# Kernel tuning notes

Measured on AMD Instinct MI355X. Metric: run time of the kernel, lower is better.

Reference implementation:

```python
import jax, jax.numpy as jnp
import numpy as np

B, S, H = 32, 512, 768          # batch, encoder seq len, hidden size
W, G = 128, 4                   # max words per example, max tokens per word group
NH, HD, FF, NL, NLAB = 4, 192, 2048, 2, 6  # heads, head dim, ffn dim, layers, labels
EPS = 1e-5


def setup_inputs() -> dict:
    key = jax.random.key(0)
    ks = jax.random.split(key, 16)
    s = 0.02
    hidden = jax.random.normal(ks[0], (B, S, H), jnp.float32)
    word_token_idx = jax.random.randint(ks[1], (B, W, G), 0, S).astype(jnp.int32)
    glen = jax.random.randint(ks[2], (B, W), 1, G + 1)
    group_token_mask = jnp.arange(G)[None, None, :] < glen[:, :, None]  # [B,W,G] bool
    nwords = jax.random.randint(ks[3], (B,), W // 2, W + 1)
    word_valid = jnp.arange(W)[None, :] < nwords[:, None]               # [B,W] bool
    return {
        'hidden': hidden,
        'word_token_idx': word_token_idx,
        'group_token_mask': group_token_mask,
        'word_valid': word_valid,
        'qkv_w': jax.random.normal(ks[4], (NL, 3 * H, H), jnp.float32) * s,
        'qkv_b': jnp.zeros((NL, 3 * H), jnp.float32),
        'out_w': jax.random.normal(ks[5], (NL, H, H), jnp.float32) * s,
        'out_b': jnp.zeros((NL, H), jnp.float32),
        'ff1_w': jax.random.normal(ks[6], (NL, FF, H), jnp.float32) * s,
        'ff1_b': jnp.zeros((NL, FF), jnp.float32),
        'ff2_w': jax.random.normal(ks[7], (NL, H, FF), jnp.float32) * s,
        'ff2_b': jnp.zeros((NL, H), jnp.float32),
        'ln1_s': jnp.ones((NL, H), jnp.float32),
        'ln1_b': jnp.zeros((NL, H), jnp.float32),
        'ln2_s': jnp.ones((NL, H), jnp.float32),
        'ln2_b': jnp.zeros((NL, H), jnp.float32),
        'cls_w': jax.random.normal(ks[8], (NLAB, H), jnp.float32) * s,
        'cls_b': jnp.zeros((NLAB,), jnp.float32),
    }


def _ln(x, s, b):
    m = x.mean(-1, keepdims=True)
    v = ((x - m) ** 2).mean(-1, keepdims=True)
    return (x - m) * jax.lax.rsqrt(v + EPS) * s + b


def reference(hidden, word_token_idx, group_token_mask, word_valid,
              qkv_w, qkv_b, out_w, out_b, ff1_w, ff1_b, ff2_w, ff2_b,
              ln1_s, ln1_b, ln2_s, ln2_b, cls_w, cls_b):
    dt = hidden.dtype
    # ragged per-word gather + masked mean over each subword group: [B,W,G,H]
    gathered = jax.vmap(lambda h, i: h[i])(hidden, word_token_idx)
    gm = group_token_mask[..., None].astype(dt)
    wemb = (gathered * gm).sum(2) / jnp.maximum(gm.sum(2), 1.0)   # [B,W,H]
    # invalid (padded) words are zero, matching torch pad_sequence zero-padding
    wemb = wemb * word_valid[..., None].astype(dt)
    cls = hidden[:, 0, :]
    x = jnp.concatenate([cls[:, None, :], wemb], axis=1)          # [B, W+1, H]
    # key padding mask: True = padded position; CLS slot always valid
    pad = jnp.concatenate([jnp.zeros((B, 1), bool), ~word_valid], axis=1)
    neg = jnp.finfo(dt).min
    Lw = W + 1
    scale = 1.0 / np.sqrt(HD)
    for l in range(NL):  # 2 post-norm TransformerEncoder layers
        qkv = x @ qkv_w[l].T + qkv_b[l]
        q, k, v = jnp.split(qkv, 3, axis=-1)
        q = q.reshape(B, Lw, NH, HD).transpose(0, 2, 1, 3)
        k = k.reshape(B, Lw, NH, HD).transpose(0, 2, 1, 3)
        v = v.reshape(B, Lw, NH, HD).transpose(0, 2, 1, 3)
        scores = jnp.einsum('bhqd,bhkd->bhqk', q, k) * scale
        scores = jnp.where(pad[:, None, None, :], neg, scores)
        a = jax.nn.softmax(scores, axis=-1)
        ctx = jnp.einsum('bhqk,bhkd->bhqd', a, v).transpose(0, 2, 1, 3).reshape(B, Lw, H)
        attn = ctx @ out_w[l].T + out_b[l]
        x = _ln(x + attn, ln1_s[l], ln1_b[l])
        h1 = jax.nn.relu(x @ ff1_w[l].T + ff1_b[l])
        x = _ln(x + h1 @ ff2_w[l].T + ff2_b[l], ln2_s[l], ln2_b[l])
    pooled = x[:, 0, :]
    logits = pooled @ cls_w.T + cls_b
    return (logits, pooled)
```

## Files before the change

kernel.cpp:

```cpp
#include <hip/hip_runtime.h>
#include <hip/hip_bf16.h>
#include <math.h>

#define B_  32
#define S_  512
#define H_  768
#define W_  128
#define G_  4
#define LW  129
#define NH_ 4
#define HD_ 192
#define FF_ 2048
#define NL_ 2
#define NLAB_ 6
#define M_   (B_ * LW)
#define MPAD 4224
#define EPS_ 1e-5f
#define SCALE_ 0.07216878364870323f

#define TP 192
#define KP 160
#define KR 144
#define KLD 200
#define PLD 168

#define QW_SZ (3 * H_ * H_)
#define OW_SZ (H_ * H_)
#define F1_SZ (FF_ * H_)
#define F2_SZ (H_ * FF_)
#define WL_SZ (QW_SZ + OW_SZ + F1_SZ + F2_SZ)

typedef __bf16 bf16_8 __attribute__((ext_vector_type(8)));
typedef float  f32x4  __attribute__((ext_vector_type(4)));
typedef unsigned short ushort8_t __attribute__((ext_vector_type(8)));

__device__ __forceinline__ float b2f(unsigned short u) {
    union { unsigned int i; float f; } c; c.i = ((unsigned int)u) << 16; return c.f;
}
__device__ __forceinline__ unsigned short f2b(float f) {
    union { float f; unsigned int u; } c; c.f = f;
    unsigned int u = c.u;
    return (unsigned short)((u + 0x7FFFu + ((u >> 16) & 1u)) >> 16);
}

__device__ __forceinline__ float wave_sum(float v) {
#pragma unroll
    for (int off = 1; off < 64; off <<= 1) v += __shfl_xor(v, off, 64);
    return v;
}
__device__ __forceinline__ float wave_max(float v) {
#pragma unroll
    for (int off = 1; off < 64; off <<= 1) v = fmaxf(v, __shfl_xor(v, off, 64));
    return v;
}
__device__ __forceinline__ float block_sum(float v, float* red) {
    v = wave_sum(v);
    int wid = threadIdx.x >> 6, lane = threadIdx.x & 63;
    if (lane == 0) red[wid] = v;
    __syncthreads();
    float r = (red[0] + red[1]) + (red[2] + red[3]);
    __syncthreads();
    return r;
}

__global__ __launch_bounds__(256) void build_cvt_kernel(
    const float* __restrict__ hidden,
    const int*   __restrict__ wti,
    const int*   __restrict__ gmask,
    const int*   __restrict__ wvalid,
    unsigned short* __restrict__ xb,
    const float4* __restrict__ qw, const float4* __restrict__ ow,
    const float4* __restrict__ f1, const float4* __restrict__ f2,
    ushort4* __restrict__ dst)
{
    int bx = blockIdx.x;
    int tid = threadIdx.x;
    if (bx >= (LW + 3) * B_) {
        constexpr int WL4 = WL_SZ / 4;
        int i = (bx - (LW + 3) * B_) * 256 + tid;
        int l = (i < WL4) ? 0 : 1;
        int j = i - l * WL4;
        float4 v;
        if (j < QW_SZ / 4)                          v = qw[l * (QW_SZ / 4) + j];
        else if (j < (QW_SZ + OW_SZ) / 4)           v = ow[l * (OW_SZ / 4) + j - QW_SZ / 4];
        else if (j < (QW_SZ + OW_SZ + F1_SZ) / 4)   v = f1[l * (F1_SZ / 4) + j - (QW_SZ + OW_SZ) / 4];
        else                                        v = f2[l * (F2_SZ / 4) + j - (QW_SZ + OW_SZ + F1_SZ) / 4];
        ushort4 o; o.x = f2b(v.x); o.y = f2b(v.y); o.z = f2b(v.z); o.w = f2b(v.w);
        dst[i] = o;
        return;
    }
    int t = bx % (LW + 3);
    int b = bx / (LW + 3);
    if (t >= LW) {
        int pr = M_ + b * 3 + (t - LW);
        size_t xo = (size_t)pr * H_;
#pragma unroll
        for (int i = 0; i < 3; i++) xb[xo + tid + i * 256] = 0;
        return;
    }
    size_t xo = ((size_t)b * LW + t) * H_;
    if (t == 0) {
        const float* src = hidden + (size_t)b * S_ * H_;
#pragma unroll
        for (int i = 0; i < 3; i++) xb[xo + tid + i * 256] = f2b(src[tid + i * 256]);
    } else {
        int w = t - 1;
        int valid = wvalid[b * W_ + w];
        int ids[G_]; float msk[G_]; float cnt = 0.f;
#pragma unroll
        for (int g = 0; g < G_; g++) {
            ids[g] = wti[(b * W_ + w) * G_ + g];
            msk[g] = (gmask[(b * W_ + w) * G_ + g] != 0) ? 1.f : 0.f;
            cnt += msk[g];
        }
        float inv = valid ? (1.f / fmaxf(cnt, 1.f)) : 0.f;
#pragma unroll
        for (int i = 0; i < 3; i++) {
            int c = tid + i * 256;
            float a = 0.f;
#pragma unroll
            for (int g = 0; g < G_; g++)
                a += msk[g] * hidden[((size_t)b * S_ + ids[g]) * H_ + c];
            xb[xo + c] = f2b(a * inv);
        }
    }
}

template <int BM, int BN, int BK, int RELU, int OUTBF, int SWZ>
__global__ __launch_bounds__(256) void gemm_mfma(
    const unsigned short* __restrict__ A,
    const unsigned short* __restrict__ Bw,
    const float* __restrict__ bias,
    void* __restrict__ Cout,
    int N, int K, int ldc, int lda)
{
    constexpr int MI  = BM / 32;
    constexpr int NJ  = BN / 32;
    constexpr int CPR = BK / 8;
    constexpr int RPL = 2048 / BK;
    constexpr int SA  = BM * BK / 2048;
    constexpr int SB  = BN * BK / 2048;

    __shared__ __align__(16) unsigned short As[BM * BK];
    __shared__ __align__(16) unsigned short Bs[BN * BK];

    const int tid  = threadIdx.x;
    const int lane = tid & 63;
    const int wid  = tid >> 6;

    int bx = blockIdx.x, by = blockIdx.y;
    if (SWZ) {
        int nx = gridDim.x;
        int total = nx * gridDim.y;
        int id = by * nx + bx;
        int id2 = (id & 7) * (total >> 3) + (id >> 3);
        by = id2 / nx; bx = id2 - by * nx;
    }
    const int bm = by * BM;
    const int bn = bx * BN;

    const int wm = (wid & 1) * (BM / 2);
    const int wn = (wid >> 1) * (BN / 2);
    const int r  = lane & 15;
    const int q8 = lane >> 4;
    const int m8 = r & (CPR - 1);

    const int srow = tid / CPR;
    const int scol = (tid % CPR) ^ (srow & (CPR - 1));
    const unsigned short* Ag = A  + (size_t)(bm + srow) * lda + scol * 8;
    const unsigned short* Bg = Bw + (size_t)(bn + srow) * K + scol * 8;

    const bf16_8* Af = (const bf16_8*)As;
    const bf16_8* Bf = (const bf16_8*)Bs;
    int arow[MI], brow[NJ];
#pragma unroll
    for (int i = 0; i < MI; i++) arow[i] = (wm + i * 16 + r) * CPR;
#pragma unroll
    for (int j = 0; j < NJ; j++) brow[j] = (wn + j * 16 + r) * CPR;

    f32x4 acc[MI][NJ];
#pragma unroll
    for (int i = 0; i < MI; i++)
#pragma unroll
        for (int j = 0; j < NJ; j++) acc[i][j] = (f32x4){0.f, 0.f, 0.f, 0.f};

    for (int k0 = 0; k0 < K; k0 += BK) {
#pragma unroll
        for (int s = 0; s < SA; s++)
            __builtin_amdgcn_global_load_lds(
                (const __attribute__((address_space(1))) void*)(Ag + (size_t)(s * RPL) * lda + k0),
                (__attribute__((address_space(3))) void*)(As + s * 2048 + tid * 8), 16, 0, 0);
#pragma unroll
        for (int s = 0; s < SB; s++)
            __builtin_amdgcn_global_load_lds(
                (const __attribute__((address_space(1))) void*)(Bg + (size_t)(s * RPL) * K + k0),
                (__attribute__((address_space(3))) void*)(Bs + s * 2048 + tid * 8), 16, 0, 0);
        __syncthreads();
#pragma unroll
        for (int ks = 0; ks < BK / 32; ks++) {
            const int cc = (ks * 4 + q8) ^ m8;
            bf16_8 a[MI], b[NJ];
#pragma unroll
            for (int i = 0; i < MI; i++) a[i] = Af[arow[i] + cc];
#pragma unroll
            for (int j = 0; j < NJ; j++) b[j] = Bf[brow[j] + cc];
#pragma unroll
            for (int i = 0; i < MI; i++)
#pragma unroll
                for (int j = 0; j < NJ; j++)
                    acc[i][j] = __builtin_amdgcn_mfma_f32_16x16x32_bf16(a[i], b[j], acc[i][j], 0, 0, 0);
        }
        __syncthreads();
    }

    int col[NJ]; float bv[NJ];
#pragma unroll
    for (int j = 0; j < NJ; j++) { col[j] = bn + wn + j * 16 + r; bv[j] = bias[col[j]]; }
    const int row0 = bm + wm + ((lane >> 4) << 2);
#pragma unroll
    for (int i = 0; i < MI; i++) {
#pragma unroll
        for (int rg = 0; rg < 4; rg++) {
            size_t rowoff = (size_t)(row0 + i * 16 + rg) * ldc;
#pragma unroll
            for (int j = 0; j < NJ; j++) {
                float v = acc[i][j][rg] + bv[j];
                if (RELU) v = fmaxf(v, 0.f);
                if (OUTBF) ((unsigned short*)Cout)[rowoff + col[j]] = f2b(v);
                else       ((float*)Cout)[rowoff + col[j]] = v;
            }
        }
    }
}

__global__ __launch_bounds__(256) void vt_kernel(
    const unsigned short* __restrict__ qkv,
    unsigned short* __restrict__ vtb)
{
    __shared__ __align__(16) unsigned short Vs[KR * KLD];
    int bh = blockIdx.x;
    int b = bh >> 2, h = bh & 3;
    int tid = threadIdx.x;
    for (int c = tid; c < KR * 24; c += 256) {
        int t = c / 24, j = c - t * 24;
        ushort8_t v = (ushort8_t){0,0,0,0,0,0,0,0};
        if (t < LW)
            v = *(const ushort8_t*)(qkv + (size_t)(b * LW + t) * (3 * H_) + 2 * H_ + h * HD_ + j * 8);
        *(ushort8_t*)(&Vs[t * KLD + j * 8]) = v;
    }
    __syncthreads();
    size_t obase = (size_t)bh * (HD_ * KP);
    for (int c = tid; c < HD_ * (KP / 4); c += 256) {
        int d = c / (KP / 4), t0 = (c - d * (KP / 4)) * 4;
        ushort4 o;
        o.x = (t0 + 0 < KR) ? Vs[(t0 + 0) * KLD + d] : 0;
        o.y = (t0 + 1 < KR) ? Vs[(t0 + 1) * KLD + d] : 0;
        o.z = (t0 + 2 < KR) ? Vs[(t0 + 2) * KLD + d] : 0;
        o.w = (t0 + 3 < KR) ? Vs[(t0 + 3) * KLD + d] : 0;
        *(ushort4*)(&vtb[obase + (size_t)d * KP + t0]) = o;
    }
}

__global__ __launch_bounds__(256) void attn_fused_kernel(
    const unsigned short* __restrict__ qkv,
    const int*            __restrict__ wvalid,
    const unsigned short* __restrict__ vtb,
    unsigned short*       __restrict__ ctx)
{
    __shared__ __align__(16) unsigned short Ks[KR * KLD];
    __shared__ __align__(16) unsigned short Ps[64 * PLD];
    __shared__ float msk[KR];
    int mb = blockIdx.x;
    int bh = blockIdx.y;
    int b = bh >> 2, h = bh & 3;
    int tid = threadIdx.x, lane = tid & 63, wid = tid >> 6;
    int q = lane >> 4, r = lane & 15;

    for (int c = tid; c < KR * 24; c += 256) {
        int t = c / 24, j = c - t * 24;
        ushort8_t v = (ushort8_t){0,0,0,0,0,0,0,0};
        if (t < LW)
            v = *(const ushort8_t*)(qkv + (size_t)(b * LW + t) * (3 * H_) + H_ + h * HD_ + j * 8);
        *(ushort8_t*)(&Ks[t * KLD + j * 8]) = v;
    }
    if (tid < KR) {
        bool valid = (tid == 0) || (tid <= W_ && wvalid[b * W_ + tid - 1] != 0);
        msk[tid] = valid ? 0.f : -1e30f;
    }
    __syncthreads();

    const int lrow0 = wid * 16;
    const unsigned short* Qp = qkv + ((size_t)(b * LW) + mb * 64 + lrow0 + r) * (3 * H_) + h * HD_;

    f32x4 acc[9];
#pragma unroll
    for (int nt = 0; nt < 9; nt++) acc[nt] = (f32x4){0.f, 0.f, 0.f, 0.f};
    for (int ks = 0; ks < HD_ / 32; ks++) {
        bf16_8 a = *(const bf16_8*)(Qp + ks * 32 + q * 8);
#pragma unroll
        for (int nt = 0; nt < 9; nt++) {
            bf16_8 bfrag = *(const bf16_8*)(&Ks[(nt * 16 + r) * KLD + ks * 32 + q * 8]);
            acc[nt] = __builtin_amdgcn_mfma_f32_16x16x32_bf16(a, bfrag, acc[nt], 0, 0, 0);
        }
    }
    float mk[9];
#pragma unroll
    for (int nt = 0; nt < 9; nt++) mk[nt] = msk[nt * 16 + r];
#pragma unroll
    for (int rg = 0; rg < 4; rg++) {
        float v[9]; float mx = -1e30f;
#pragma unroll
        for (int nt = 0; nt < 9; nt++) { v[nt] = acc[nt][rg] * SCALE_ + mk[nt]; mx = fmaxf(mx, v[nt]); }
#pragma unroll
        for (int off = 1; off < 16; off <<= 1) mx = fmaxf(mx, __shfl_xor(mx, off, 64));
        float s = 0.f;
#pragma unroll
        for (int nt = 0; nt < 9; nt++) { v[nt] = __expf(v[nt] - mx); s += v[nt]; }
#pragma unroll
        for (int off = 1; off < 16; off <<= 1) s += __shfl_xor(s, off, 64);
        float inv = 1.f / s;
        int lr = lrow0 + q * 4 + rg;
#pragma unroll
        for (int nt = 0; nt < 9; nt++)
            Ps[lr * PLD + nt * 16 + r] = f2b(v[nt] * inv);
        Ps[lr * PLD + KR + r] = 0;
    }
    __syncthreads();

    const int wm = (wid & 1) * 32, wn = (wid >> 1) * 96;
    size_t vbase = (size_t)bh * (HD_ * KP);

    f32x4 pacc[2][6];
#pragma unroll
    for (int i = 0; i < 2; i++)
#pragma unroll
        for (int j = 0; j < 6; j++) pacc[i][j] = (f32x4){0.f, 0.f, 0.f, 0.f};

    for (int ks = 0; ks < KP / 32; ks++) {
        bf16_8 a[2], bb[6];
#pragma unroll
        for (int i = 0; i < 2; i++)
            a[i] = *(const bf16_8*)(&Ps[(wm + i * 16 + r) * PLD + ks * 32 + q * 8]);
#pragma unroll
        for (int j = 0; j < 6; j++)
            bb[j] = *(const bf16_8*)(vtb + vbase + (size_t)(wn + j * 16 + r) * KP + ks * 32 + q * 8);
#pragma unroll
        for (int i = 0; i < 2; i++)
#pragma unroll
            for (int j = 0; j < 6; j++)
                pacc[i][j] = __builtin_amdgcn_mfma_f32_16x16x32_bf16(a[i], bb[j], pacc[i][j], 0, 0, 0);
    }

#pragma unroll
    for (int i = 0; i < 2; i++) {
#pragma unroll
        for (int rg = 0; rg < 4; rg++) {
            int tl = mb * 64 + wm + i * 16 + q * 4 + rg;
            if (tl < LW) {
                size_t rowoff = (size_t)(b * LW + tl) * H_ + h * HD_;
#pragma unroll
                for (int j = 0; j < 6; j++)
                    ctx[rowoff + wn + j * 16 + r] = f2b(pacc[i][j][rg]);
            }
        }
    }
}

__global__ __launch_bounds__(256) void add_ln_kernel(
    unsigned short* __restrict__ xb, const unsigned short* __restrict__ res,
    const float* __restrict__ sc, const float* __restrict__ bi)
{
    __shared__ float red[4];
    int row = blockIdx.x;
    int tid = threadIdx.x;
    size_t base = (size_t)row * H_;
    float v[3];
    float sum = 0.f;
#pragma unroll
    for (int i = 0; i < 3; i++) {
        int c = tid + i * 256;
        float t = b2f(xb[base + c]) + b2f(res[base + c]);
        v[i] = t; sum += t;
    }
    sum = block_sum(sum, red);
    float mean = sum * (1.f / H_);
    float var = 0.f;
#pragma unroll
    for (int i = 0; i < 3; i++) { float d = v[i] - mean; var += d * d; }
    var = block_sum(var, red);
    float inv = rsqrtf(var * (1.f / H_) + EPS_);
#pragma unroll
    for (int i = 0; i < 3; i++) {
        int c = tid + i * 256;
        xb[base + c] = f2b((v[i] - mean) * inv * sc[c] + bi[c]);
    }
}

__global__ __launch_bounds__(256) void cls_attn_core2_kernel(
    const unsigned short* __restrict__ qrows,
    const unsigned short* __restrict__ qkvb,
    const int* __restrict__ wvalid,
    unsigned short* __restrict__ ctxc)
{
    __shared__ float qh[HD_];
    __shared__ float ps[LW];
    __shared__ float red[4];
    int b = blockIdx.x, h = blockIdx.y;
    int tid = threadIdx.x, lane = tid & 63, wid = tid >> 6;
    if (tid < HD_) qh[tid] = b2f(qrows[(size_t)b * H_ + h * HD_ + tid]);
    __syncthreads();
    float sc = -1e30f;
    if (tid < LW) {
        const unsigned short* kr = qkvb + (size_t)(b * LW + tid) * (3 * H_) + H_ + h * HD_;
        float acc = 0.f;
#pragma unroll
        for (int j = 0; j < HD_ / 8; j++) {
            ushort8_t k8 = *(const ushort8_t*)(kr + j * 8);
#pragma unroll
            for (int jj = 0; jj < 8; jj++) acc += qh[j * 8 + jj] * b2f(k8[jj]);
        }
        bool valid = (tid == 0) || (wvalid[b * W_ + tid - 1] != 0);
        sc = valid ? acc * SCALE_ : -1e30f;
    }
    float mx = wave_max(sc);
    if (lane == 0) red[wid] = mx;
    __syncthreads();
    mx = fmaxf(fmaxf(red[0], red[1]), fmaxf(red[2], red[3]));
    __syncthreads();
    float e = (tid < LW) ? __expf(sc - mx) : 0.f;
    float ssum = wave_sum(e);
    if (lane == 0) red[wid] = ssum;
    __syncthreads();
    ssum = (red[0] + red[1]) + (red[2] + red[3]);
    if (tid < LW) ps[tid] = e * (1.f / ssum);
    __syncthreads();
    if (tid < HD_) {
        const unsigned short* vb = qkvb + (size_t)(b * LW) * (3 * H_) + 2 * H_ + h * HD_ + tid;
        float cx = 0.f;
#pragma unroll 8
        for (int t = 0; t < LW; t++)
            cx += ps[t] * b2f(vb[(size_t)t * (3 * H_)]);
        ctxc[(size_t)b * H_ + h * HD_ + tid] = f2b(cx);
    }
}

__global__ __launch_bounds__(256) void cls_ln1_kernel(
    const unsigned short* __restrict__ proj,
    const unsigned short* __restrict__ xb,
    const float* __restrict__ sc, const float* __restrict__ bi,
    unsigned short* __restrict__ dst)
{
    __shared__ float red[4];
    int b = blockIdx.x;
    int tid = threadIdx.x;
    float v[3]; float sum = 0.f;
#pragma unroll
    for (int i = 0; i < 3; i++) {
        int c = tid + i * 256;
        float t = b2f(proj[(size_t)b * H_ + c]) + b2f(xb[(size_t)(b * LW) * H_ + c]);
        v[i] = t; sum += t;
    }
    sum = block_sum(sum, red);
    float mean = sum * (1.f / H_);
    float var = 0.f;
#pragma unroll
    for (int i = 0; i < 3; i++) { float d = v[i] - mean; var += d * d; }
    var = block_sum(var, red);
    float inv = rsqrtf(var * (1.f / H_) + EPS_);
#pragma unroll
    for (int i = 0; i < 3; i++) {
        int c = tid + i * 256;
        dst[(size_t)b * H_ + c] = f2b((v[i] - mean) * inv * sc[c] + bi[c]);
    }
}

__global__ __launch_bounds__(256) void cls_final_kernel(
    const unsigned short* __restrict__ proj,
    const unsigned short* __restrict__ resid,
    const float* __restrict__ ln2s, const float* __restrict__ ln2b,
    const float* __restrict__ cls_w, const float* __restrict__ cls_b,
    float* __restrict__ out)
{
    __shared__ float red[4];
    __shared__ float lred[4][NLAB_];
    int b = blockIdx.x;
    int tid = threadIdx.x, lane = tid & 63, wid = tid >> 6;
    size_t base = (size_t)b * H_;
    float v[3]; float sum = 0.f;
#pragma unroll
    for (int i = 0; i < 3; i++) {
        int c = tid + i * 256;
        float t = b2f(proj[base + c]) + b2f(resid[base + c]);
        v[i] = t; sum += t;
    }
    sum = block_sum(sum, red);
    float mean = sum * (1.f / H_);
    float var = 0.f;
#pragma unroll
    for (int i = 0; i < 3; i++) { float d = v[i] - mean; var += d * d; }
    var = block_sum(var, red);
    float rinv = rsqrtf(var * (1.f / H_) + EPS_);
    float f3[3];
#pragma unroll
    for (int i = 0; i < 3; i++) {
        int c = tid + i * 256;
        f3[i] = (v[i] - mean) * rinv * ln2s[c] + ln2b[c];
        out[B_ * NLAB_ + b * H_ + c] = f3[i];
    }
    float l6[NLAB_] = {0.f, 0.f, 0.f, 0.f, 0.f, 0.f};
#pragma unroll
    for (int i = 0; i < 3; i++) {
        int c = tid + i * 256;
#pragma unroll
        for (int w = 0; w < NLAB_; w++) l6[w] += f3[i] * cls_w[w * H_ + c];
    }
#pragma unroll
    for (int w = 0; w < NLAB_; w++) l6[w] = wave_sum(l6[w]);
    if (lane == 0) {
#pragma unroll
        for (int w = 0; w < NLAB_; w++) lred[wid][w] = l6[w];
    }
    __syncthreads();
    if (tid < NLAB_)
        out[b * NLAB_ + tid] = lred[0][tid] + lred[1][tid] + lred[2][tid] + lred[3][tid] + cls_b[tid];
}

extern "C" void kernel_launch(void* const* d_in, const int* in_sizes, int n_in,
                              void* d_out, int out_size, void* d_ws, size_t ws_size,
                              hipStream_t stream) {
    const float* hidden = (const float*)d_in[0];
    const int*   wti    = (const int*)d_in[1];
    const int*   gmask  = (const int*)d_in[2];
    const int*   wvalid = (const int*)d_in[3];
    const float* qkv_w  = (const float*)d_in[4];
    const float* qkv_b  = (const float*)d_in[5];
    const float* out_w  = (const float*)d_in[6];
    const float* out_b  = (const float*)d_in[7];
    const float* ff1_w  = (const float*)d_in[8];
    const float* ff1_b  = (const float*)d_in[9];
    const float* ff2_w  = (const float*)d_in[10];
    const float* ff2_b  = (const float*)d_in[11];
    const float* ln1_s  = (const float*)d_in[12];
    const float* ln1_b  = (const float*)d_in[13];
    const float* ln2_s  = (const float*)d_in[14];
    const float* ln2_b  = (const float*)d_in[15];
    const float* cls_w  = (const float*)d_in[16];
    const float* cls_b  = (const float*)d_in[17];
    float* out = (float*)d_out;

    const size_t XSZ = (size_t)MPAD * H_;
    const size_t ASZ = (size_t)128 * TP * KP;
    const size_t R64 = (size_t)64 * H_;
    unsigned short* U    = (unsigned short*)d_ws;
    unsigned short* vtb  = U;
    unsigned short* tmpb = U;
    unsigned short* qrows64 = U + 1 * R64;
    unsigned short* ctxc  = U + 2 * R64;
    unsigned short* xc64  = U + 3 * R64;
    unsigned short* tmp64 = U + 4 * R64;
    unsigned short* h1c   = U + 5 * R64;
    unsigned short* xb   = U + ASZ;
    unsigned short* ctxb = xb + XSZ;
    unsigned short* qkvb = ctxb + XSZ;
    unsigned short* wb   = qkvb + (size_t)MPAD * 3 * H_;

    build_cvt_kernel<<<(LW + 3) * B_ + 2 * WL_SZ / 4 / 256, 256, 0, stream>>>(
        hidden, wti, gmask, wvalid, xb,
        (const float4*)qkv_w, (const float4*)out_w,
        (const float4*)ff1_w, (const float4*)ff2_w, (ushort4*)wb);

    const int GM = MPAD / 64;

    {
        unsigned short* wbl = wb;
        gemm_mfma<64, 128, 64, 0, 1, 0><<<dim3(3 * H_ / 128, GM), 256, 0, stream>>>(
            xb, wbl, qkv_b, qkvb, 3 * H_, H_, 3 * H_, H_);
        vt_kernel<<<128, 256, 0, stream>>>(qkvb, vtb);
        attn_fused_kernel<<<dim3(3, 128), 256, 0, stream>>>(qkvb, wvalid, vtb, ctxb);
        gemm_mfma<64, 64, 64, 0, 1, 1><<<dim3(H_ / 64, GM), 256, 0, stream>>>(
            ctxb, wbl + QW_SZ, out_b, tmpb, H_, H_, H_, H_);
        add_ln_kernel<<<M_, 256, 0, stream>>>(xb, tmpb, ln1_s, ln1_b);
        gemm_mfma<64, 128, 64, 1, 1, 1><<<dim3(FF_ / 128, GM), 256, 0, stream>>>(
            xb, wbl + QW_SZ + OW_SZ, ff1_b, qkvb, FF_, H_, FF_, H_);
        gemm_mfma<64, 64, 64, 0, 1, 1><<<dim3(H_ / 64, GM), 256, 0, stream>>>(
            qkvb, wbl + QW_SZ + OW_SZ + F1_SZ, ff2_b, tmpb, H_, FF_, H_, FF_);
        add_ln_kernel<<<M_, 256, 0, stream>>>(xb, tmpb, ln2_s, ln2_b);
    }

    {
        unsigned short* wbl = wb + WL_SZ;
        gemm_mfma<64, 128, 64, 0, 1, 1><<<dim3(1536 / 128, GM), 256, 0, stream>>>(
            xb, wbl + (size_t)H_ * H_, qkv_b + 3 * H_ + H_, qkvb + H_, 2 * H_, H_, 3 * H_, H_);
        gemm_mfma<64, 128, 64, 0, 1, 0><<<dim3(H_ / 128, 1), 256, 0, stream>>>(
            xb, wbl, qkv_b + 3 * H_, qrows64, H_, H_, H_, LW * H_);
        cls_attn_core2_kernel<<<dim3(B_, NH_), 256, 0, stream>>>(
            qrows64, qkvb, wvalid, ctxc);
        gemm_mfma<64, 128, 64, 0, 1, 0><<<dim3(H_ / 128, 1), 256, 0, stream>>>(
            ctxc, wbl + QW_SZ, out_b + H_, tmp64, H_, H_, H_, H_);
        cls_ln1_kernel<<<B_, 256, 0, stream>>>(tmp64, xb, ln1_s + H_, ln1_b + H_, xc64);
        gemm_mfma<64, 128, 64, 1, 1, 0><<<dim3(FF_ / 128, 1), 256, 0, stream>>>(
            xc64, wbl + QW_SZ + OW_SZ, ff1_b + FF_, h1c, FF_, H_, FF_, H_);
        gemm_mfma<64, 128, 64, 0, 1, 0><<<dim3(H_ / 128, 1), 256, 0, stream>>>(
            h1c, wbl + QW_SZ + OW_SZ + F1_SZ, ff2_b + H_, tmp64, H_, FF_, H_, FF_);
        cls_final_kernel<<<B_, 256, 0, stream>>>(tmp64, xc64, ln2_s + H_, ln2_b + H_,
                                                 cls_w, cls_b, out);
    }
    (void)in_sizes; (void)n_in; (void)out_size; (void)ws_size;
}
```

Baseline: 377.6 us.

## Fuse last-layer KV and CLS-Q GEMMs, skip padded attention rows, parallelize CLS scores

Merges the last layer's K/V projection GEMM and the CLS query projection into one launch by adding an extra grid column that computes the query rows. In the fused attention kernel, waves whose query rows lie entirely past the 129-token sequence now skip the score/softmax and PV work. The CLS attention kernel spreads each key dot product across 8 threads with shuffle reductions instead of one thread per key. Together these aim to cut a launch, wasted padded-row compute, and serial per-thread dot products, at the cost of hardcoded grid constants (792, 12, 13) in the fused GEMM.

```diff
diff --git a/kernel.cpp b/kernel.cpp
--- a/kernel.cpp
+++ b/kernel.cpp
@@ -126,6 +126,100 @@
     }
 }
 
+template <int BM, int BN, int BK, int RELU, int OUTBF>
+__device__ __forceinline__ void gemm_body(
+    unsigned short* As, unsigned short* Bs,
+    const unsigned short* __restrict__ A,
+    const unsigned short* __restrict__ Bw,
+    const float* __restrict__ bias,
+    void* __restrict__ Cout,
+    int N, int K, int ldc, int lda, int bm, int bn)
+{
+    constexpr int MI  = BM / 32;
+    constexpr int NJ  = BN / 32;
+    constexpr int CPR = BK / 8;
+    constexpr int RPL = 2048 / BK;
+    constexpr int SA  = BM * BK / 2048;
+    constexpr int SB  = BN * BK / 2048;
+
+    const int tid  = threadIdx.x;
+    const int lane = tid & 63;
+    const int wid  = tid >> 6;
+
+    const int wm = (wid & 1) * (BM / 2);
+    const int wn = (wid >> 1) * (BN / 2);
+    const int r  = lane & 15;
+    const int q8 = lane >> 4;
+    const int m8 = r & (CPR - 1);
+
+    const int srow = tid / CPR;
+    const int scol = (tid % CPR) ^ (srow & (CPR - 1));
+    const unsigned short* Ag = A  + (size_t)(bm + srow) * lda + scol * 8;
+    const unsigned short* Bg = Bw + (size_t)(bn + srow) * K + scol * 8;
+
+    const bf16_8* Af = (const bf16_8*)As;
+    const bf16_8* Bf = (const bf16_8*)Bs;
+    int arow[MI], brow[NJ];
+#pragma unroll
+    for (int i = 0; i < MI; i++) arow[i] = (wm + i * 16 + r) * CPR;
+#pragma unroll
+    for (int j = 0; j < NJ; j++) brow[j] = (wn + j * 16 + r) * CPR;
+
+    f32x4 acc[MI][NJ];
+#pragma unroll
+    for (int i = 0; i < MI; i++)
+#pragma unroll
+        for (int j = 0; j < NJ; j++) acc[i][j] = (f32x4){0.f, 0.f, 0.f, 0.f};
+
+    for (int k0 = 0; k0 < K; k0 += BK) {
+#pragma unroll
+        for (int s = 0; s < SA; s++)
+            __builtin_amdgcn_global_load_lds(
+                (const __attribute__((address_space(1))) void*)(Ag + (size_t)(s * RPL) * lda + k0),
+                (__attribute__((address_space(3))) void*)(As + s * 2048 + tid * 8), 16, 0, 0);
+#pragma unroll
+        for (int s = 0; s < SB; s++)
+            __builtin_amdgcn_global_load_lds(
+                (const __attribute__((address_space(1))) void*)(Bg + (size_t)(s * RPL) * K + k0),
+                (__attribute__((address_space(3))) void*)(Bs + s * 2048 + tid * 8), 16, 0, 0);
+        __syncthreads();
+#pragma unroll
+        for (int ks = 0; ks < BK / 32; ks++) {
+            const int cc = (ks * 4 + q8) ^ m8;
+            bf16_8 a[MI], b[NJ];
+#pragma unroll
+            for (int i = 0; i < MI; i++) a[i] = Af[arow[i] + cc];
+#pragma unroll
+            for (int j = 0; j < NJ; j++) b[j] = Bf[brow[j] + cc];
+#pragma unroll
+            for (int i = 0; i < MI; i++)
+#pragma unroll
+                for (int j = 0; j < NJ; j++)
+                    acc[i][j] = __builtin_amdgcn_mfma_f32_16x16x32_bf16(a[i], b[j], acc[i][j], 0, 0, 0);
+        }
+        __syncthreads();
+    }
+
+    int col[NJ]; float bv[NJ];
+#pragma unroll
+    for (int j = 0; j < NJ; j++) { col[j] = bn + wn + j * 16 + r; bv[j] = bias[col[j]]; }
+    const int row0 = bm + wm + ((lane >> 4) << 2);
+#pragma unroll
+    for (int i = 0; i < MI; i++) {
+#pragma unroll
+        for (int rg = 0; rg < 4; rg++) {
+            size_t rowoff = (size_t)(row0 + i * 16 + rg) * ldc;
+#pragma unroll
+            for (int j = 0; j < NJ; j++) {
+                float v = acc[i][j][rg] + bv[j];
+                if (RELU) v = fmaxf(v, 0.f);
+                if (OUTBF) ((unsigned short*)Cout)[rowoff + col[j]] = f2b(v);
+                else       ((float*)Cout)[rowoff + col[j]] = v;
+            }
+        }
+    }
+}
+
 template <int BM, int BN, int BK, int RELU, int OUTBF, int SWZ>
 __global__ __launch_bounds__(256) void gemm_mfma(
     const unsigned short* __restrict__ A,
@@ -134,20 +228,8 @@
     void* __restrict__ Cout,
     int N, int K, int ldc, int lda)
 {
-    constexpr int MI  = BM / 32;
-    constexpr int NJ  = BN / 32;
-    constexpr int CPR = BK / 8;
-    constexpr int RPL = 2048 / BK;
-    constexpr int SA  = BM * BK / 2048;
-    constexpr int SB  = BN * BK / 2048;
-
     __shared__ __align__(16) unsigned short As[BM * BK];
     __shared__ __align__(16) unsigned short Bs[BN * BK];
-
-    const int tid  = threadIdx.x;
-    const int lane = tid & 63;
-    const int wid  = tid >> 6;
-
     int bx = blockIdx.x, by = blockIdx.y;
     if (SWZ) {
         int nx = gridDim.x;
@@ -156,81 +238,33 @@
         int id2 = (id & 7) * (total >> 3) + (id >> 3);
         by = id2 / nx; bx = id2 - by * nx;
     }
-    const int bm = by * BM;
-    const int bn = bx * BN;
-
-    const int wm = (wid & 1) * (BM / 2);
-    const int wn = (wid >> 1) * (BN / 2);
-    const int r  = lane & 15;
-    const int q8 = lane >> 4;
-    const int m8 = r & (CPR - 1);
-
-    const int srow = tid / CPR;
-    const int scol = (tid % CPR) ^ (srow & (CPR - 1));
-    const unsigned short* Ag = A  + (size_t)(bm + srow) * lda + scol * 8;
-    const unsigned short* Bg = Bw + (size_t)(bn + srow) * K + scol * 8;
-
-    const bf16_8* Af = (const bf16_8*)As;
-    const bf16_8* Bf = (const bf16_8*)Bs;
-    int arow[MI], brow[NJ];
-#pragma unroll
-    for (int i = 0; i < MI; i++) arow[i] = (wm + i * 16 + r) * CPR;
-#pragma unroll
-    for (int j = 0; j < NJ; j++) brow[j] = (wn + j * 16 + r) * CPR;
-
-    f32x4 acc[MI][NJ];
-#pragma unroll
-    for (int i = 0; i < MI; i++)
-#pragma unroll
-        for (int j = 0; j < NJ; j++) acc[i][j] = (f32x4){0.f, 0.f, 0.f, 0.f};
-
-    for (int k0 = 0; k0 < K; k0 += BK) {
-#pragma unroll
-        for (int s = 0; s < SA; s++)
-            __builtin_amdgcn_global_load_lds(
-                (const __attribute__((address_space(1))) void*)(Ag + (size_t)(s * RPL) * lda + k0),
-                (__attribute__((address_space(3))) void*)(As + s * 2048 + tid * 8), 16, 0, 0);
-#pragma unroll
-        for (int s = 0; s < SB; s++)
-            __builtin_amdgcn_global_load_lds(
-                (const __attribute__((address_space(1))) void*)(Bg + (size_t)(s * RPL) * K + k0),
-                (__attribute__((address_space(3))) void*)(Bs + s * 2048 + tid * 8), 16, 0, 0);
-        __syncthreads();
-#pragma unroll
-        for (int ks = 0; ks < BK / 32; ks++) {
-            const int cc = (ks * 4 + q8) ^ m8;
-            bf16_8 a[MI], b[NJ];
-#pragma unroll
-            for (int i = 0; i < MI; i++) a[i] = Af[arow[i] + cc];
-#pragma unroll
-            for (int j = 0; j < NJ; j++) b[j] = Bf[brow[j] + cc];
-#pragma unroll
-            for (int i = 0; i < MI; i++)
-#pragma unroll
-                for (int j = 0; j < NJ; j++)
-                    acc[i][j] = __builtin_amdgcn_mfma_f32_16x16x32_bf16(a[i], b[j], acc[i][j], 0, 0, 0);
-        }
-        __syncthreads();
-    }
-
-    int col[NJ]; float bv[NJ];
-#pragma unroll
-    for (int j = 0; j < NJ; j++) { col[j] = bn + wn + j * 16 + r; bv[j] = bias[col[j]]; }
-    const int row0 = bm + wm + ((lane >> 4) << 2);
-#pragma unroll
-    for (int i = 0; i < MI; i++) {
-#pragma unroll
-        for (int rg = 0; rg < 4; rg++) {
-            size_t rowoff = (size_t)(row0 + i * 16 + rg) * ldc;
-#pragma unroll
-            for (int j = 0; j < NJ; j++) {
-                float v = acc[i][j][rg] + bv[j];
-                if (RELU) v = fmaxf(v, 0.f);
-                if (OUTBF) ((unsigned short*)Cout)[rowoff + col[j]] = f2b(v);
-                else       ((float*)Cout)[rowoff + col[j]] = v;
-            }
-        }
-    }
+    gemm_body<BM, BN, BK, RELU, OUTBF>(As, Bs, A, Bw, bias, Cout, N, K, ldc, lda,
+                                       by * BM, bx * BN);
+}
+
+__global__ __launch_bounds__(256) void gemm_kv_q_kernel(
+    const unsigned short* __restrict__ xb,
+    const unsigned short* __restrict__ wkv,
+    const float* __restrict__ bkv,
+    unsigned short* __restrict__ kvout,
+    const unsigned short* __restrict__ wq,
+    const float* __restrict__ qb,
+    unsigned short* __restrict__ qrows)
+{
+    __shared__ __align__(16) unsigned short As[64 * 64];
+    __shared__ __align__(16) unsigned short Bs[128 * 64];
+    int bx = blockIdx.x, by = blockIdx.y;
+    if (bx == 12) {
+        if (by >= 6) return;
+        gemm_body<64, 128, 64, 0, 1>(As, Bs, xb, wq, qb, qrows,
+                                     H_, H_, H_, LW * H_, 0, by * 128);
+        return;
+    }
+    int id = by * 12 + bx;
+    int id2 = (id & 7) * (792 >> 3) + (id >> 3);
+    by = id2 / 12; bx = id2 - by * 12;
+    gemm_body<64, 128, 64, 0, 1>(As, Bs, xb, wkv, bkv, kvout,
+                                 2 * H_, H_, 3 * H_, H_, by * 64, bx * 128);
 }
 
 __global__ __launch_bounds__(256) void vt_kernel(
@@ -290,77 +324,80 @@
     __syncthreads();
 
     const int lrow0 = wid * 16;
-    const unsigned short* Qp = qkv + ((size_t)(b * LW) + mb * 64 + lrow0 + r) * (3 * H_) + h * HD_;
-
-    f32x4 acc[9];
-#pragma unroll
-    for (int nt = 0; nt < 9; nt++) acc[nt] = (f32x4){0.f, 0.f, 0.f, 0.f};
-    for (int ks = 0; ks < HD_ / 32; ks++) {
-        bf16_8 a = *(const bf16_8*)(Qp + ks * 32 + q * 8);
-#pragma unroll
-        for (int nt = 0; nt < 9; nt++) {
-            bf16_8 bfrag = *(const bf16_8*)(&Ks[(nt * 16 + r) * KLD + ks * 32 + q * 8]);
-            acc[nt] = __builtin_amdgcn_mfma_f32_16x16x32_bf16(a, bfrag, acc[nt], 0, 0, 0);
-        }
-    }
-    float mk[9];
-#pragma unroll
-    for (int nt = 0; nt < 9; nt++) mk[nt] = msk[nt * 16 + r];
-#pragma unroll
-    for (int rg = 0; rg < 4; rg++) {
-        float v[9]; float mx = -1e30f;
-#pragma unroll
-        for (int nt = 0; nt < 9; nt++) { v[nt] = acc[nt][rg] * SCALE_ + mk[nt]; mx = fmaxf(mx, v[nt]); }
-#pragma unroll
-        for (int off = 1; off < 16; off <<= 1) mx = fmaxf(mx, __shfl_xor(mx, off, 64));
-        float s = 0.f;
-#pragma unroll
-        for (int nt = 0; nt < 9; nt++) { v[nt] = __expf(v[nt] - mx); s += v[nt]; }
-#pragma unroll
-        for (int off = 1; off < 16; off <<= 1) s += __shfl_xor(s, off, 64);
-        float inv = 1.f / s;
-        int lr = lrow0 + q * 4 + rg;
-#pragma unroll
-        for (int nt = 0; nt < 9; nt++)
-            Ps[lr * PLD + nt * 16 + r] = f2b(v[nt] * inv);
-        Ps[lr * PLD + KR + r] = 0;
+    const bool p1_active = (mb < 2) || (lrow0 == 0);
+    if (p1_active) {
+        const unsigned short* Qp = qkv + ((size_t)(b * LW) + mb * 64 + lrow0 + r) * (3 * H_) + h * HD_;
+        f32x4 acc[9];
+#pragma unroll
+        for (int nt = 0; nt < 9; nt++) acc[nt] = (f32x4){0.f, 0.f, 0.f, 0.f};
+        for (int ks = 0; ks < HD_ / 32; ks++) {
+            bf16_8 a = *(const bf16_8*)(Qp + ks * 32 + q * 8);
+#pragma unroll
+            for (int nt = 0; nt < 9; nt++) {
+                bf16_8 bfrag = *(const bf16_8*)(&Ks[(nt * 16 + r) * KLD + ks * 32 + q * 8]);
+                acc[nt] = __builtin_amdgcn_mfma_f32_16x16x32_bf16(a, bfrag, acc[nt], 0, 0, 0);
+            }
+        }
+        float mk[9];
+#pragma unroll
+        for (int nt = 0; nt < 9; nt++) mk[nt] = msk[nt * 16 + r];
+#pragma unroll
+        for (int rg = 0; rg < 4; rg++) {
+            float v[9]; float mx = -1e30f;
+#pragma unroll
+            for (int nt = 0; nt < 9; nt++) { v[nt] = acc[nt][rg] * SCALE_ + mk[nt]; mx = fmaxf(mx, v[nt]); }
+#pragma unroll
+            for (int off = 1; off < 16; off <<= 1) mx = fmaxf(mx, __shfl_xor(mx, off, 64));
+            float s = 0.f;
+#pragma unroll
+            for (int nt = 0; nt < 9; nt++) { v[nt] = __expf(v[nt] - mx); s += v[nt]; }
+#pragma unroll
+            for (int off = 1; off < 16; off <<= 1) s += __shfl_xor(s, off, 64);
+            float inv = 1.f / s;
+            int lr = lrow0 + q * 4 + rg;
+#pragma unroll
+            for (int nt = 0; nt < 9; nt++)
+                Ps[lr * PLD + nt * 16 + r] = f2b(v[nt] * inv);
+            Ps[lr * PLD + KR + r] = 0;
+        }
     }
     __syncthreads();
 
     const int wm = (wid & 1) * 32, wn = (wid >> 1) * 96;
-    size_t vbase = (size_t)bh * (HD_ * KP);
-
-    f32x4 pacc[2][6];
-#pragma unroll
-    for (int i = 0; i < 2; i++)
-#pragma unroll
-        for (int j = 0; j < 6; j++) pacc[i][j] = (f32x4){0.f, 0.f, 0.f, 0.f};
-
-    for (int ks = 0; ks < KP / 32; ks++) {
-        bf16_8 a[2], bb[6];
+    if (!(mb == 2 && wm == 32)) {
+        size_t vbase = (size_t)bh * (HD_ * KP);
+        f32x4 pacc[2][6];
 #pragma unroll
         for (int i = 0; i < 2; i++)
-            a[i] = *(const bf16_8*)(&Ps[(wm + i * 16 + r) * PLD + ks * 32 + q * 8]);
-#pragma unroll
-        for (int j = 0; j < 6; j++)
-            bb[j] = *(const bf16_8*)(vtb + vbase + (size_t)(wn + j * 16 + r) * KP + ks * 32 + q * 8);
-#pragma unroll
-        for (int i = 0; i < 2; i++)
+#pragma unroll
+            for (int j = 0; j < 6; j++) pacc[i][j] = (f32x4){0.f, 0.f, 0.f, 0.f};
+
+        for (int ks = 0; ks < KP / 32; ks++) {
+            bf16_8 a[2], bb[6];
+#pragma unroll
+            for (int i = 0; i < 2; i++)
+                a[i] = *(const bf16_8*)(&Ps[(wm + i * 16 + r) * PLD + ks * 32 + q * 8]);
 #pragma unroll
             for (int j = 0; j < 6; j++)
-                pacc[i][j] = __builtin_amdgcn_mfma_f32_16x16x32_bf16(a[i], bb[j], pacc[i][j], 0, 0, 0);
-    }
-
-#pragma unroll
-    for (int i = 0; i < 2; i++) {
-#pragma unroll
-        for (int rg = 0; rg < 4; rg++) {
-            int tl = mb * 64 + wm + i * 16 + q * 4 + rg;
-            if (tl < LW) {
-                size_t rowoff = (size_t)(b * LW + tl) * H_ + h * HD_;
+                bb[j] = *(const bf16_8*)(vtb + vbase + (size_t)(wn + j * 16 + r) * KP + ks * 32 + q * 8);
+#pragma unroll
+            for (int i = 0; i < 2; i++)
 #pragma unroll
                 for (int j = 0; j < 6; j++)
-                    ctx[rowoff + wn + j * 16 + r] = f2b(pacc[i][j][rg]);
+                    pacc[i][j] = __builtin_amdgcn_mfma_f32_16x16x32_bf16(a[i], bb[j], pacc[i][j], 0, 0, 0);
+        }
+
+#pragma unroll
+        for (int i = 0; i < 2; i++) {
+#pragma unroll
+            for (int rg = 0; rg < 4; rg++) {
+                int tl = mb * 64 + wm + i * 16 + q * 4 + rg;
+                if (tl < LW) {
+                    size_t rowoff = (size_t)(b * LW + tl) * H_ + h * HD_;
+#pragma unroll
+                    for (int j = 0; j < 6; j++)
+                        ctx[rowoff + wn + j * 16 + r] = f2b(pacc[i][j][rg]);
+                }
             }
         }
     }
@@ -403,25 +440,37 @@
     unsigned short* __restrict__ ctxc)
 {
     __shared__ float qh[HD_];
+    __shared__ float sr[160];
     __shared__ float ps[LW];
     __shared__ float red[4];
     int b = blockIdx.x, h = blockIdx.y;
     int tid = threadIdx.x, lane = tid & 63, wid = tid >> 6;
     if (tid < HD_) qh[tid] = b2f(qrows[(size_t)b * H_ + h * HD_ + tid]);
     __syncthreads();
-    float sc = -1e30f;
-    if (tid < LW) {
-        const unsigned short* kr = qkvb + (size_t)(b * LW + tid) * (3 * H_) + H_ + h * HD_;
+    int grp = tid >> 3, s8 = tid & 7;
+#pragma unroll
+    for (int p = 0; p < 5; p++) {
+        int t = p * 32 + grp;
         float acc = 0.f;
-#pragma unroll
-        for (int j = 0; j < HD_ / 8; j++) {
-            ushort8_t k8 = *(const ushort8_t*)(kr + j * 8);
-#pragma unroll
-            for (int jj = 0; jj < 8; jj++) acc += qh[j * 8 + jj] * b2f(k8[jj]);
-        }
-        bool valid = (tid == 0) || (wvalid[b * W_ + tid - 1] != 0);
-        sc = valid ? acc * SCALE_ : -1e30f;
-    }
+        if (t < LW) {
+            const unsigned short* kr = qkvb + (size_t)(b * LW + t) * (3 * H_) + H_ + h * HD_ + s8 * 24;
+#pragma unroll
+            for (int j = 0; j < 3; j++) {
+                ushort8_t k8 = *(const ushort8_t*)(kr + j * 8);
+#pragma unroll
+                for (int jj = 0; jj < 8; jj++) acc += qh[s8 * 24 + j * 8 + jj] * b2f(k8[jj]);
+            }
+        }
+        acc += __shfl_xor(acc, 1, 64);
+        acc += __shfl_xor(acc, 2, 64);
+        acc += __shfl_xor(acc, 4, 64);
+        if (s8 == 0 && t < LW) {
+            bool valid = (t == 0) || (wvalid[b * W_ + t - 1] != 0);
+            sr[t] = valid ? acc * SCALE_ : -1e30f;
+        }
+    }
+    __syncthreads();
+    float sc = (tid < LW) ? sr[tid] : -1e30f;
     float mx = wave_max(sc);
     if (lane == 0) red[wid] = mx;
     __syncthreads();
@@ -589,10 +638,9 @@
 
     {
         unsigned short* wbl = wb + WL_SZ;
-        gemm_mfma<64, 128, 64, 0, 1, 1><<<dim3(1536 / 128, GM), 256, 0, stream>>>(
-            xb, wbl + (size_t)H_ * H_, qkv_b + 3 * H_ + H_, qkvb + H_, 2 * H_, H_, 3 * H_, H_);
-        gemm_mfma<64, 128, 64, 0, 1, 0><<<dim3(H_ / 128, 1), 256, 0, stream>>>(
-            xb, wbl, qkv_b + 3 * H_, qrows64, H_, H_, H_, LW * H_);
+        gemm_kv_q_kernel<<<dim3(13, GM), 256, 0, stream>>>(
+            xb, wbl + (size_t)H_ * H_, qkv_b + 3 * H_ + H_, qkvb + H_,
+            wbl, qkv_b + 3 * H_, qrows64);
         cls_attn_core2_kernel<<<dim3(B_, NH_), 256, 0, stream>>>(
             qrows64, qkvb, wvalid, ctxc);
         gemm_mfma<64, 128, 64, 0, 1, 0><<<dim3(H_ / 128, 1), 256, 0, stream>>>(
```

New measurement: 376.6 us. About the same (-0.3%).
